# Kernel tuning notes

Measured on AMD Instinct MI355X. Metric: run time of the kernel, lower is better.

Reference implementation:

```python
import jax, jax.numpy as jnp
import numpy as np

N_TREES, DEPTH, INPUT_DIM, N_CLASSES = 15, 3, 128, 10
N_LEAVES = 2 ** DEPTH
N_INTERNAL = N_LEAVES - 1


def _path_masks(depth):
    """Right/left ancestor indicator matrices [n_leaves, n_internal]."""
    n_leaves = 2 ** depth
    n_int = n_leaves - 1
    R = np.zeros((n_leaves, n_int), np.float32)
    L = np.zeros((n_leaves, n_int), np.float32)
    for leaf in range(n_leaves):
        node = leaf + n_int
        for _ in range(depth):
            parent = (node - 1) // 2
            if node % 2 == 0:
                R[leaf, parent] = 1.0
            else:
                L[leaf, parent] = 1.0
            node = parent
    return R, L

_R, _L = _path_masks(DEPTH)


def setup_inputs() -> dict:
    key = jax.random.key(0)
    k1, k2 = jax.random.split(key)
    batch = 262144
    per_tree = N_INTERNAL * INPUT_DIM + N_INTERNAL + N_LEAVES * N_CLASSES
    total = N_TREES * per_tree + N_TREES
    x = jax.random.normal(k1, (batch, INPUT_DIM), dtype=jnp.float32)
    params = jax.random.normal(k2, (total,), dtype=jnp.float32)
    return {"x": x, "params": params}


def reference(x, params):
    per_tree = N_INTERNAL * INPUT_DIM + N_INTERNAL + N_LEAVES * N_CLASSES
    blocks = params[: N_TREES * per_tree].reshape(N_TREES, per_tree)
    w_end = N_INTERNAL * INPUT_DIM
    split_w = blocks[:, :w_end].reshape(N_TREES, N_INTERNAL, INPUT_DIM)
    split_b = blocks[:, w_end : w_end + N_INTERNAL]  # [T, n_internal]
    leaf_logits = blocks[:, w_end + N_INTERNAL :].reshape(N_TREES, N_LEAVES, N_CLASSES)
    tree_w_logits = params[N_TREES * per_tree :]  # [T]

    # split logits z: [B, T, n_internal]
    z = jnp.einsum("bd,tnd->btn", x, split_w) + split_b[None, :, :]
    log_p = jax.nn.log_sigmoid(z)        # log sigma(z)
    log_1mp = jax.nn.log_sigmoid(-z)     # log (1 - sigma(z))

    R = jnp.asarray(_R)
    L = jnp.asarray(_L)
    # path product in log domain: [B, T, n_leaves]
    leaf_probs = jnp.exp(
        jnp.einsum("btn,ln->btl", log_p, R) + jnp.einsum("btn,ln->btl", log_1mp, L)
    )

    leaf_class_probs = jax.nn.softmax(leaf_logits, axis=-1)  # [T, n_leaves, C]
    tree_pred = jnp.einsum("btl,tlc->btc", leaf_probs, leaf_class_probs)
    tree_weights = jax.nn.softmax(tree_w_logits, axis=0)     # [T]
    final_pred = jnp.einsum("btc,t->bc", tree_pred, tree_weights)
    return final_pred
```

## Files before the change

### kernel.cpp

```cpp
#include <hip/hip_runtime.h>
#include <hip/hip_fp16.h>


typedef float    f32x4 __attribute__((ext_vector_type(4)));
typedef _Float16 half8 __attribute__((ext_vector_type(8)));

#define TREES      15
#define IDIM       128
#define NCLS       10
#define NINT       7
#define NLVS       8
#define PER_TREE   (NINT*IDIM + NINT + NLVS*NCLS)
#define NODES      (TREES*NINT)
#define NPAD       112
#define KPAD       128
#define RSTR       272
#define NBLK       512

__global__ __launch_bounds__(256) void prep_kernel(const float* __restrict__ p,
                                                   _Float16* __restrict__ wq,
                                                   float* __restrict__ bq,
                                                   _Float16* __restrict__ wbT) {
    const int gid  = blockIdx.x * 256 + threadIdx.x;
    const int nthr = gridDim.x * 256;

    for (int i = gid; i < NPAD * IDIM; i += nthr) {
        int g = i >> 7, k = i & 127;
        float v = 0.f;
        if (g < NODES) {
            int t = g / NINT, n = g % NINT;
            v = p[t * PER_TREE + n * IDIM + k];
        }
        wq[i] = (_Float16)v;
    }
    for (int i = gid; i < NPAD; i += nthr) {
        float v = 0.f;
        if (i < NODES) {
            int t = i / NINT, n = i % NINT;
            v = p[t * PER_TREE + NINT * IDIM + n];
        }
        bq[i] = v;
    }
    const float* tl = p + TREES * PER_TREE;
    for (int i = gid; i < 16 * KPAD; i += nthr) {
        int c = i >> 7, k = i & 127;
        float v = 0.f;
        if (c < NCLS && k < TREES * NLVS) {
            int t = k >> 3, l = k & 7;
            const float* ll = p + t * PER_TREE + NINT * IDIM + NINT + l * NCLS;
            float mx = ll[0];
            #pragma unroll
            for (int j = 1; j < NCLS; ++j) mx = fmaxf(mx, ll[j]);
            float se = 0.f;
            #pragma unroll
            for (int j = 0; j < NCLS; ++j) se += __expf(ll[j] - mx);
            float lsm = __expf(ll[c] - mx) / se;

            float m2 = tl[0];
            #pragma unroll
            for (int j = 1; j < TREES; ++j) m2 = fmaxf(m2, tl[j]);
            float s2 = 0.f;
            #pragma unroll
            for (int j = 0; j < TREES; ++j) s2 += __expf(tl[j] - m2);
            float tw = __expf(tl[t] - m2) / s2;
            v = lsm * tw;
        }
        wbT[i] = (_Float16)v;
    }
}

__device__ __forceinline__ void dma_quarter(const float* __restrict__ x,
                                            long grow0, char* qdst, int lane) {
    #pragma unroll
    for (int it = 0; it < 8; ++it) {
        int r = 2 * it + (lane >> 5);
        const float* gp = x + (grow0 + r) * IDIM + (lane & 31) * 4;
        __builtin_amdgcn_global_load_lds(
            (const __attribute__((address_space(1))) void*)gp,
            (__attribute__((address_space(3))) void*)(qdst + it * 1024),
            16, 0, 0);
    }
}

__global__ __launch_bounds__(256, 2) void tree_main(const float* __restrict__ x,
                                                    const _Float16* __restrict__ wq,
                                                    const float* __restrict__ bq,
                                                    const _Float16* __restrict__ wbT,
                                                    float* __restrict__ out,
                                                    int tpb) {
    __shared__ __align__(16) char lds[2][32768];

    const int tid  = threadIdx.x;
    const int lane = tid & 63;
    const int w    = tid >> 6;
    const int lm   = lane & 15;
    const int lq   = lane >> 4;
    const int rg   = lane >> 2;
    const int g    = lane & 3;

    const long tile0 = (long)blockIdx.x * tpb;

    dma_quarter(x, tile0 * 64 + 16 * w, &lds[0][w * 8192], lane);

    half8 bf[7][4];
    float bb[7];
    #pragma unroll
    for (int nt = 0; nt < 7; ++nt) {
        bb[nt] = bq[16 * nt + lm];
        #pragma unroll
        for (int s = 0; s < 4; ++s)
            bf[nt][s] = *reinterpret_cast<const half8*>(wq + (16 * nt + lm) * IDIM + 32 * s + 8 * lq);
    }
    half8 wbf[4];
    #pragma unroll
    for (int s = 0; s < 4; ++s)
        wbf[s] = *reinterpret_cast<const half8*>(wbT + lm * KPAD + 32 * s + 8 * lq);

    asm volatile("" ::: "memory");
    __builtin_amdgcn_s_waitcnt(0x0F70);
    asm volatile("" ::: "memory");
    if (tpb > 1)
        dma_quarter(x, (tile0 + 1) * 64 + 16 * w, &lds[1][w * 8192], lane);

    for (int i = 0; i < tpb; ++i) {
        char* qcur = &lds[i & 1][w * 8192];
        const long grow = (tile0 + i) * 64;

        asm volatile("" ::: "memory");
        if (i == 1)                __builtin_amdgcn_s_waitcnt(0x0F7C);
        else if (i >= 2 && i < tpb - 1)
                                   __builtin_amdgcn_s_waitcnt(0x4F70);
        else if (i == tpb - 1 && i >= 2)
                                   __builtin_amdgcn_s_waitcnt(0x0F78);
        asm volatile("" ::: "memory");

        half8 af[4];
        #pragma unroll
        for (int s = 0; s < 4; ++s) {
            int cc = 8 * s + 2 * lq;
            f32x4 f0 = *(const f32x4*)(qcur + lm * 512 + (cc     << 4));
            f32x4 f1 = *(const f32x4*)(qcur + lm * 512 + ((cc + 1) << 4));
            half8 a;
            #pragma unroll
            for (int j = 0; j < 4; ++j) {
                a[j]     = (_Float16)f0[j];
                a[j + 4] = (_Float16)f1[j];
            }
            af[s] = a;
        }

        #pragma unroll
        for (int nt = 0; nt < 7; ++nt) {
            f32x4 acc = {bb[nt], bb[nt], bb[nt], bb[nt]};
            #pragma unroll
            for (int s = 0; s < 4; ++s)
                acc = __builtin_amdgcn_mfma_f32_16x16x32_f16(af[s], bf[nt][s], acc, 0, 0, 0);
            int node = 16 * nt + lm;
            int col  = node + ((node * 9363) >> 16);
            #pragma unroll
            for (int r = 0; r < 4; ++r) {
                float z  = acc[r];
                float sg = __builtin_amdgcn_rcpf(1.0f + __expf(-z));
                *(_Float16*)(qcur + (4 * lq + r) * RSTR + col * 2) = (_Float16)sg;
            }
        }

        {
            const char* rowp = qcur + rg * RSTR;
            half8 hv[4];
            #pragma unroll
            for (int tt = 0; tt < 4; ++tt)
                hv[tt] = *(const half8*)(rowp + 64 * g + 16 * tt);
            half8 lv[4];
            #pragma unroll
            for (int tt = 0; tt < 4; ++tt) {
                float s0 = (float)hv[tt][0], s1 = (float)hv[tt][1], s2v = (float)hv[tt][2];
                float s3 = (float)hv[tt][3], s4 = (float)hv[tt][4], s5 = (float)hv[tt][5];
                float s6 = (float)hv[tt][6];
                float u1 = 1.f - s0, u2 = s0;
                float q1 = u1 * s1, q0 = u1 - q1;
                float q3 = u2 * s2v, q2 = u2 - q3;
                float L1 = q0 * s3, L0 = q0 - L1;
                float L3 = q1 * s4, L2 = q1 - L3;
                float L5 = q2 * s5, L4 = q2 - L5;
                float L7 = q3 * s6, L6 = q3 - L7;
                float m = (4 * g + tt < TREES) ? 1.f : 0.f;
                half8 lv8;
                lv8[0] = (_Float16)(L0 * m); lv8[1] = (_Float16)(L1 * m);
                lv8[2] = (_Float16)(L2 * m); lv8[3] = (_Float16)(L3 * m);
                lv8[4] = (_Float16)(L4 * m); lv8[5] = (_Float16)(L5 * m);
                lv8[6] = (_Float16)(L6 * m); lv8[7] = (_Float16)(L7 * m);
                lv[tt] = lv8;
            }
            #pragma unroll
            for (int tt = 0; tt < 4; ++tt)
                *(half8*)(qcur + rg * RSTR + 64 * g + 16 * tt) = lv[tt];
        }

        {
            half8 af2[4];
            #pragma unroll
            for (int s = 0; s < 4; ++s)
                af2[s] = *(const half8*)(qcur + lm * RSTR + 64 * s + 16 * lq);
            f32x4 a2 = {0.f, 0.f, 0.f, 0.f};
            #pragma unroll
            for (int s = 0; s < 4; ++s)
                a2 = __builtin_amdgcn_mfma_f32_16x16x32_f16(af2[s], wbf[s], a2, 0, 0, 0);

            asm volatile("" ::: "memory");
            if (i + 2 < tpb)
                dma_quarter(x, (tile0 + i + 2) * 64 + 16 * w, qcur, lane);
            asm volatile("" ::: "memory");

            if (lm < NCLS) {
                #pragma unroll
                for (int r = 0; r < 4; ++r)
                    out[(grow + 16 * w + 4 * lq + r) * NCLS + lm] = a2[r];
            }
        }
    }
}

extern "C" void kernel_launch(void* const* d_in, const int* in_sizes, int n_in,
                              void* d_out, int out_size, void* d_ws, size_t ws_size,
                              hipStream_t stream) {
    const float* x      = (const float*)d_in[0];
    const float* params = (const float*)d_in[1];
    float* out = (float*)d_out;

    _Float16* wq  = (_Float16*)d_ws;
    float*    bq  = (float*)((char*)d_ws + NPAD * IDIM * 2);
    _Float16* wbT = (_Float16*)((char*)bq + NPAD * 4);

    const int batch = in_sizes[0] / IDIM;
    const int tiles = batch / 64;
    const int tpb   = tiles / NBLK;

    prep_kernel<<<8, 256, 0, stream>>>(params, wq, bq, wbT);
    tree_main<<<NBLK, 256, 0, stream>>>(x, wq, bq, wbT, out, tpb);
}
```

Before: 202.1 us.

## Replace persistent double-buffered loop with one-tile-per-block grid and streamed weights

The persistent kernel, where 512 blocks loop over tiles with double-buffered async LDS loads, becomes a non-persistent launch with one 64-row tile per block and a single LDS buffer. Split weights are no longer held in registers for the whole kernel. They are streamed per node tile with a one-step register prefetch, which lowers register pressure, and launch bounds are raised to 4 blocks per CU. This trades the explicit load/compute overlap for occupancy-based latency hiding. It also adds per-block weight reloads from L2 and per-block launch overhead across 4096 blocks.

```diff
diff --git a/kernel.cpp b/kernel.cpp
--- a/kernel.cpp
+++ b/kernel.cpp
@@ -15,7 +15,6 @@
 #define NPAD       112
 #define KPAD       128
 #define RSTR       272
-#define NBLK       512
 
 __global__ __launch_bounds__(256) void prep_kernel(const float* __restrict__ p,
                                                    _Float16* __restrict__ wq,
@@ -82,13 +81,12 @@
     }
 }
 
-__global__ __launch_bounds__(256, 2) void tree_main(const float* __restrict__ x,
+__global__ __launch_bounds__(256, 4) void tree_main(const float* __restrict__ x,
                                                     const _Float16* __restrict__ wq,
                                                     const float* __restrict__ bq,
                                                     const _Float16* __restrict__ wbT,
-                                                    float* __restrict__ out,
-                                                    int tpb) {
-    __shared__ __align__(16) char lds[2][32768];
+                                                    float* __restrict__ out) {
+    __shared__ __align__(16) char lds[32768];
 
     const int tid  = threadIdx.x;
     const int lane = tid & 63;
@@ -98,125 +96,116 @@
     const int rg   = lane >> 2;
     const int g    = lane & 3;
 
-    const long tile0 = (long)blockIdx.x * tpb;
-
-    dma_quarter(x, tile0 * 64 + 16 * w, &lds[0][w * 8192], lane);
-
-    half8 bf[7][4];
-    float bb[7];
-    #pragma unroll
-    for (int nt = 0; nt < 7; ++nt) {
-        bb[nt] = bq[16 * nt + lm];
-        #pragma unroll
-        for (int s = 0; s < 4; ++s)
-            bf[nt][s] = *reinterpret_cast<const half8*>(wq + (16 * nt + lm) * IDIM + 32 * s + 8 * lq);
-    }
+    char* qcur = &lds[w * 8192];
+    const long grow = (long)blockIdx.x * 64;
+
+    dma_quarter(x, grow + 16 * w, qcur, lane);
+
     half8 wbf[4];
     #pragma unroll
     for (int s = 0; s < 4; ++s)
         wbf[s] = *reinterpret_cast<const half8*>(wbT + lm * KPAD + 32 * s + 8 * lq);
 
+    half8 bfc[4], bfn[4];
+    float bbc, bbn;
+    {
+        const _Float16* wp = wq + lm * IDIM;
+        #pragma unroll
+        for (int s = 0; s < 4; ++s)
+            bfc[s] = *reinterpret_cast<const half8*>(wp + 32 * s + 8 * lq);
+        bbc = bq[lm];
+    }
+
     asm volatile("" ::: "memory");
     __builtin_amdgcn_s_waitcnt(0x0F70);
     asm volatile("" ::: "memory");
-    if (tpb > 1)
-        dma_quarter(x, (tile0 + 1) * 64 + 16 * w, &lds[1][w * 8192], lane);
-
-    for (int i = 0; i < tpb; ++i) {
-        char* qcur = &lds[i & 1][w * 8192];
-        const long grow = (tile0 + i) * 64;
-
-        asm volatile("" ::: "memory");
-        if (i == 1)                __builtin_amdgcn_s_waitcnt(0x0F7C);
-        else if (i >= 2 && i < tpb - 1)
-                                   __builtin_amdgcn_s_waitcnt(0x4F70);
-        else if (i == tpb - 1 && i >= 2)
-                                   __builtin_amdgcn_s_waitcnt(0x0F78);
-        asm volatile("" ::: "memory");
-
-        half8 af[4];
-        #pragma unroll
-        for (int s = 0; s < 4; ++s) {
-            int cc = 8 * s + 2 * lq;
-            f32x4 f0 = *(const f32x4*)(qcur + lm * 512 + (cc     << 4));
-            f32x4 f1 = *(const f32x4*)(qcur + lm * 512 + ((cc + 1) << 4));
-            half8 a;
-            #pragma unroll
-            for (int j = 0; j < 4; ++j) {
-                a[j]     = (_Float16)f0[j];
-                a[j + 4] = (_Float16)f1[j];
-            }
-            af[s] = a;
-        }
-
-        #pragma unroll
-        for (int nt = 0; nt < 7; ++nt) {
-            f32x4 acc = {bb[nt], bb[nt], bb[nt], bb[nt]};
+
+    half8 af[4];
+    #pragma unroll
+    for (int s = 0; s < 4; ++s) {
+        int cc = 8 * s + 2 * lq;
+        f32x4 f0 = *(const f32x4*)(qcur + lm * 512 + (cc       << 4));
+        f32x4 f1 = *(const f32x4*)(qcur + lm * 512 + ((cc + 1) << 4));
+        half8 a;
+        #pragma unroll
+        for (int j = 0; j < 4; ++j) {
+            a[j]     = (_Float16)f0[j];
+            a[j + 4] = (_Float16)f1[j];
+        }
+        af[s] = a;
+    }
+
+    #pragma unroll 1
+    for (int nt = 0; nt < 7; ++nt) {
+        if (nt + 1 < 7) {
+            const _Float16* wp = wq + (16 * (nt + 1) + lm) * IDIM;
             #pragma unroll
             for (int s = 0; s < 4; ++s)
-                acc = __builtin_amdgcn_mfma_f32_16x16x32_f16(af[s], bf[nt][s], acc, 0, 0, 0);
-            int node = 16 * nt + lm;
-            int col  = node + ((node * 9363) >> 16);
-            #pragma unroll
-            for (int r = 0; r < 4; ++r) {
-                float z  = acc[r];
-                float sg = __builtin_amdgcn_rcpf(1.0f + __expf(-z));
-                *(_Float16*)(qcur + (4 * lq + r) * RSTR + col * 2) = (_Float16)sg;
-            }
-        }
-
-        {
-            const char* rowp = qcur + rg * RSTR;
-            half8 hv[4];
-            #pragma unroll
-            for (int tt = 0; tt < 4; ++tt)
-                hv[tt] = *(const half8*)(rowp + 64 * g + 16 * tt);
-            half8 lv[4];
-            #pragma unroll
-            for (int tt = 0; tt < 4; ++tt) {
-                float s0 = (float)hv[tt][0], s1 = (float)hv[tt][1], s2v = (float)hv[tt][2];
-                float s3 = (float)hv[tt][3], s4 = (float)hv[tt][4], s5 = (float)hv[tt][5];
-                float s6 = (float)hv[tt][6];
-                float u1 = 1.f - s0, u2 = s0;
-                float q1 = u1 * s1, q0 = u1 - q1;
-                float q3 = u2 * s2v, q2 = u2 - q3;
-                float L1 = q0 * s3, L0 = q0 - L1;
-                float L3 = q1 * s4, L2 = q1 - L3;
-                float L5 = q2 * s5, L4 = q2 - L5;
-                float L7 = q3 * s6, L6 = q3 - L7;
-                float m = (4 * g + tt < TREES) ? 1.f : 0.f;
-                half8 lv8;
-                lv8[0] = (_Float16)(L0 * m); lv8[1] = (_Float16)(L1 * m);
-                lv8[2] = (_Float16)(L2 * m); lv8[3] = (_Float16)(L3 * m);
-                lv8[4] = (_Float16)(L4 * m); lv8[5] = (_Float16)(L5 * m);
-                lv8[6] = (_Float16)(L6 * m); lv8[7] = (_Float16)(L7 * m);
-                lv[tt] = lv8;
-            }
-            #pragma unroll
-            for (int tt = 0; tt < 4; ++tt)
-                *(half8*)(qcur + rg * RSTR + 64 * g + 16 * tt) = lv[tt];
-        }
-
-        {
-            half8 af2[4];
-            #pragma unroll
-            for (int s = 0; s < 4; ++s)
-                af2[s] = *(const half8*)(qcur + lm * RSTR + 64 * s + 16 * lq);
-            f32x4 a2 = {0.f, 0.f, 0.f, 0.f};
-            #pragma unroll
-            for (int s = 0; s < 4; ++s)
-                a2 = __builtin_amdgcn_mfma_f32_16x16x32_f16(af2[s], wbf[s], a2, 0, 0, 0);
-
-            asm volatile("" ::: "memory");
-            if (i + 2 < tpb)
-                dma_quarter(x, (tile0 + i + 2) * 64 + 16 * w, qcur, lane);
-            asm volatile("" ::: "memory");
-
-            if (lm < NCLS) {
-                #pragma unroll
-                for (int r = 0; r < 4; ++r)
-                    out[(grow + 16 * w + 4 * lq + r) * NCLS + lm] = a2[r];
-            }
+                bfn[s] = *reinterpret_cast<const half8*>(wp + 32 * s + 8 * lq);
+            bbn = bq[16 * (nt + 1) + lm];
+        }
+        f32x4 acc = {bbc, bbc, bbc, bbc};
+        #pragma unroll
+        for (int s = 0; s < 4; ++s)
+            acc = __builtin_amdgcn_mfma_f32_16x16x32_f16(af[s], bfc[s], acc, 0, 0, 0);
+        int node = 16 * nt + lm;
+        int col  = node + ((node * 9363) >> 16);
+        #pragma unroll
+        for (int r = 0; r < 4; ++r) {
+            float z  = acc[r];
+            float sg = __builtin_amdgcn_rcpf(1.0f + __expf(-z));
+            *(_Float16*)(qcur + (4 * lq + r) * RSTR + col * 2) = (_Float16)sg;
+        }
+        #pragma unroll
+        for (int s = 0; s < 4; ++s) bfc[s] = bfn[s];
+        bbc = bbn;
+    }
+
+    {
+        const char* rowp = qcur + rg * RSTR;
+        half8 hv[4];
+        #pragma unroll
+        for (int tt = 0; tt < 4; ++tt)
+            hv[tt] = *(const half8*)(rowp + 64 * g + 16 * tt);
+        half8 lv[4];
+        #pragma unroll
+        for (int tt = 0; tt < 4; ++tt) {
+            float s0 = (float)hv[tt][0], s1 = (float)hv[tt][1], s2v = (float)hv[tt][2];
+            float s3 = (float)hv[tt][3], s4 = (float)hv[tt][4], s5 = (float)hv[tt][5];
+            float s6 = (float)hv[tt][6];
+            float u1 = 1.f - s0, u2 = s0;
+            float q1 = u1 * s1, q0 = u1 - q1;
+            float q3 = u2 * s2v, q2 = u2 - q3;
+            float L1 = q0 * s3, L0 = q0 - L1;
+            float L3 = q1 * s4, L2 = q1 - L3;
+            float L5 = q2 * s5, L4 = q2 - L5;
+            float L7 = q3 * s6, L6 = q3 - L7;
+            float m = (4 * g + tt < TREES) ? 1.f : 0.f;
+            half8 lv8;
+            lv8[0] = (_Float16)(L0 * m); lv8[1] = (_Float16)(L1 * m);
+            lv8[2] = (_Float16)(L2 * m); lv8[3] = (_Float16)(L3 * m);
+            lv8[4] = (_Float16)(L4 * m); lv8[5] = (_Float16)(L5 * m);
+            lv8[6] = (_Float16)(L6 * m); lv8[7] = (_Float16)(L7 * m);
+            lv[tt] = lv8;
+        }
+        #pragma unroll
+        for (int tt = 0; tt < 4; ++tt)
+            *(half8*)(qcur + rg * RSTR + 64 * g + 16 * tt) = lv[tt];
+    }
+
+    {
+        half8 af2[4];
+        #pragma unroll
+        for (int s = 0; s < 4; ++s)
+            af2[s] = *(const half8*)(qcur + lm * RSTR + 64 * s + 16 * lq);
+        f32x4 a2 = {0.f, 0.f, 0.f, 0.f};
+        #pragma unroll
+        for (int s = 0; s < 4; ++s)
+            a2 = __builtin_amdgcn_mfma_f32_16x16x32_f16(af2[s], wbf[s], a2, 0, 0, 0);
+        if (lm < NCLS) {
+            #pragma unroll
+            for (int r = 0; r < 4; ++r)
+                out[(grow + 16 * w + 4 * lq + r) * NCLS + lm] = a2[r];
         }
     }
 }
@@ -234,8 +223,7 @@
 
     const int batch = in_sizes[0] / IDIM;
     const int tiles = batch / 64;
-    const int tpb   = tiles / NBLK;
 
     prep_kernel<<<8, 256, 0, stream>>>(params, wq, bq, wbT);
-    tree_main<<<NBLK, 256, 0, stream>>>(x, wq, bq, wbT, out, tpb);
-}
+    tree_main<<<tiles, 256, 0, stream>>>(x, wq, bq, wbT, out);
+}
```

New measurement: 225.4 us. 11.5% more time.

## Fuse parameter prep into main kernel, staging converted weights through LDS

Applied to the files above, without the earlier changes.

Removes the separate prep kernel launch and has each block convert the split weights, biases and softmax-weighted leaf matrix directly from params into the second LDS buffer, then load MFMA fragments from there. This drops one launch and the global round-trip through the workspace. In exchange, every one of the 512 blocks redundantly recomputes the prep work (roughly 14K weight conversions plus softmaxes) before its main loop, and two barriers are added.

```diff
diff --git a/kernel.cpp b/kernel.cpp
--- a/kernel.cpp
+++ b/kernel.cpp
@@ -17,58 +17,6 @@
 #define RSTR       272
 #define NBLK       512
 
-__global__ __launch_bounds__(256) void prep_kernel(const float* __restrict__ p,
-                                                   _Float16* __restrict__ wq,
-                                                   float* __restrict__ bq,
-                                                   _Float16* __restrict__ wbT) {
-    const int gid  = blockIdx.x * 256 + threadIdx.x;
-    const int nthr = gridDim.x * 256;
-
-    for (int i = gid; i < NPAD * IDIM; i += nthr) {
-        int g = i >> 7, k = i & 127;
-        float v = 0.f;
-        if (g < NODES) {
-            int t = g / NINT, n = g % NINT;
-            v = p[t * PER_TREE + n * IDIM + k];
-        }
-        wq[i] = (_Float16)v;
-    }
-    for (int i = gid; i < NPAD; i += nthr) {
-        float v = 0.f;
-        if (i < NODES) {
-            int t = i / NINT, n = i % NINT;
-            v = p[t * PER_TREE + NINT * IDIM + n];
-        }
-        bq[i] = v;
-    }
-    const float* tl = p + TREES * PER_TREE;
-    for (int i = gid; i < 16 * KPAD; i += nthr) {
-        int c = i >> 7, k = i & 127;
-        float v = 0.f;
-        if (c < NCLS && k < TREES * NLVS) {
-            int t = k >> 3, l = k & 7;
-            const float* ll = p + t * PER_TREE + NINT * IDIM + NINT + l * NCLS;
-            float mx = ll[0];
-            #pragma unroll
-            for (int j = 1; j < NCLS; ++j) mx = fmaxf(mx, ll[j]);
-            float se = 0.f;
-            #pragma unroll
-            for (int j = 0; j < NCLS; ++j) se += __expf(ll[j] - mx);
-            float lsm = __expf(ll[c] - mx) / se;
-
-            float m2 = tl[0];
-            #pragma unroll
-            for (int j = 1; j < TREES; ++j) m2 = fmaxf(m2, tl[j]);
-            float s2 = 0.f;
-            #pragma unroll
-            for (int j = 0; j < TREES; ++j) s2 += __expf(tl[j] - m2);
-            float tw = __expf(tl[t] - m2) / s2;
-            v = lsm * tw;
-        }
-        wbT[i] = (_Float16)v;
-    }
-}
-
 __device__ __forceinline__ void dma_quarter(const float* __restrict__ x,
                                             long grow0, char* qdst, int lane) {
     #pragma unroll
@@ -83,9 +31,7 @@
 }
 
 __global__ __launch_bounds__(256, 2) void tree_main(const float* __restrict__ x,
-                                                    const _Float16* __restrict__ wq,
-                                                    const float* __restrict__ bq,
-                                                    const _Float16* __restrict__ wbT,
+                                                    const float* __restrict__ p,
                                                     float* __restrict__ out,
                                                     int tpb) {
     __shared__ __align__(16) char lds[2][32768];
@@ -102,19 +48,74 @@
 
     dma_quarter(x, tile0 * 64 + 16 * w, &lds[0][w * 8192], lane);
 
+    _Float16* wqs = (_Float16*)&lds[1][0];
+    _Float16* wbs = (_Float16*)&lds[1][28672];
+
+    for (int i2 = tid; i2 < NPAD * IDIM; i2 += 256) {
+        int g2 = i2 >> 7, k = i2 & 127;
+        float v = 0.f;
+        if (g2 < NODES) {
+            int t = (g2 * 9363) >> 16;
+            int n = g2 - 7 * t;
+            v = p[t * PER_TREE + n * IDIM + k];
+        }
+        wqs[i2] = (_Float16)v;
+    }
+    {
+        const float* tl = p + TREES * PER_TREE;
+        float m2 = tl[0];
+        #pragma unroll
+        for (int j = 1; j < TREES; ++j) m2 = fmaxf(m2, tl[j]);
+        float s2 = 0.f;
+        #pragma unroll
+        for (int j = 0; j < TREES; ++j) s2 += __expf(tl[j] - m2);
+        for (int i2 = tid; i2 < 16 * KPAD; i2 += 256) {
+            int c = i2 >> 7, k = i2 & 127;
+            float v = 0.f;
+            if (c < NCLS && k < TREES * NLVS) {
+                int t = k >> 3, l = k & 7;
+                const float* ll = p + t * PER_TREE + NINT * IDIM + NINT + l * NCLS;
+                float mx = ll[0];
+                #pragma unroll
+                for (int j = 1; j < NCLS; ++j) mx = fmaxf(mx, ll[j]);
+                float se = 0.f;
+                #pragma unroll
+                for (int j = 0; j < NCLS; ++j) se += __expf(ll[j] - mx);
+                float lsm = __expf(ll[c] - mx) / se;
+                float tw  = __expf(tl[t] - m2) / s2;
+                v = lsm * tw;
+            }
+            wbs[i2] = (_Float16)v;
+        }
+    }
+
+    float bb[7];
+    #pragma unroll
+    for (int nt = 0; nt < 7; ++nt) {
+        int node = 16 * nt + lm;
+        float v = 0.f;
+        if (node < NODES) {
+            int t = (node * 9363) >> 16;
+            int n = node - 7 * t;
+            v = p[t * PER_TREE + NINT * IDIM + n];
+        }
+        bb[nt] = v;
+    }
+
+    __syncthreads();
+
     half8 bf[7][4];
-    float bb[7];
-    #pragma unroll
-    for (int nt = 0; nt < 7; ++nt) {
-        bb[nt] = bq[16 * nt + lm];
+    #pragma unroll
+    for (int nt = 0; nt < 7; ++nt)
         #pragma unroll
         for (int s = 0; s < 4; ++s)
-            bf[nt][s] = *reinterpret_cast<const half8*>(wq + (16 * nt + lm) * IDIM + 32 * s + 8 * lq);
-    }
+            bf[nt][s] = *reinterpret_cast<const half8*>(wqs + (16 * nt + lm) * IDIM + 32 * s + 8 * lq);
     half8 wbf[4];
     #pragma unroll
     for (int s = 0; s < 4; ++s)
-        wbf[s] = *reinterpret_cast<const half8*>(wbT + lm * KPAD + 32 * s + 8 * lq);
+        wbf[s] = *reinterpret_cast<const half8*>(wbs + lm * KPAD + 32 * s + 8 * lq);
+
+    __syncthreads();
 
     asm volatile("" ::: "memory");
     __builtin_amdgcn_s_waitcnt(0x0F70);
@@ -138,7 +139,7 @@
         #pragma unroll
         for (int s = 0; s < 4; ++s) {
             int cc = 8 * s + 2 * lq;
-            f32x4 f0 = *(const f32x4*)(qcur + lm * 512 + (cc     << 4));
+            f32x4 f0 = *(const f32x4*)(qcur + lm * 512 + (cc       << 4));
             f32x4 f1 = *(const f32x4*)(qcur + lm * 512 + ((cc + 1) << 4));
             half8 a;
             #pragma unroll
@@ -228,14 +229,9 @@
     const float* params = (const float*)d_in[1];
     float* out = (float*)d_out;
 
-    _Float16* wq  = (_Float16*)d_ws;
-    float*    bq  = (float*)((char*)d_ws + NPAD * IDIM * 2);
-    _Float16* wbT = (_Float16*)((char*)bq + NPAD * 4);
-
     const int batch = in_sizes[0] / IDIM;
     const int tiles = batch / 64;
     const int tpb   = tiles / NBLK;
 
-    prep_kernel<<<8, 256, 0, stream>>>(params, wq, bq, wbT);
-    tree_main<<<NBLK, 256, 0, stream>>>(x, wq, bq, wbT, out, tpb);
+    tree_main<<<NBLK, 256, 0, stream>>>(x, params, out, tpb);
 }
```

Measured after the change: 219.4 us. 8.5% more time.
